# Kernel tuning notes

Measured on AMD Instinct MI355X. Metric: run time of the kernel, lower is better.

Reference implementation:

```python
import jax, jax.numpy as jnp
import numpy as np

TOP_K = 2
POOL = 4  # EfficientSpatialRouter.pool_scale


def silu(v):
    return v * jax.nn.sigmoid(v)


def setup_inputs() -> dict:
    key = jax.random.key(0)
    ks = jax.random.split(key, 6)
    B, C, H, W = 16, 256, 56, 56
    E, O = 4, 256
    hidden = 2 * C            # SimpleExpert expand_ratio=2
    red = max(C // 8, 8)      # router reduced_channels
    x = jax.random.normal(ks[0], (B, C, H, W), jnp.float32)
    router_w1 = jax.random.normal(ks[1], (red, C, 3, 3), jnp.float32) * 0.02
    router_w2 = jax.random.normal(ks[2], (E, red), jnp.float32) * 0.01
    expert_w1 = jax.random.normal(ks[3], (E, hidden, C), jnp.float32) * 0.05
    expert_w2 = jax.random.normal(ks[4], (E, O, hidden), jnp.float32) * 0.03
    shared_w = jax.random.normal(ks[5], (O, C), jnp.float32) * 0.05
    return {"x": x, "router_w1": router_w1, "router_w2": router_w2,
            "expert_w1": expert_w1, "expert_w2": expert_w2, "shared_w": shared_w}


def reference(x, router_w1, router_w2, expert_w1, expert_w2, shared_w):
    # Eval mode: no router noise; BatchNorm with default running stats
    # (mean=0, var=1, gamma=1, beta=0) is the identity, so BNs are omitted.
    B, C, H, W = x.shape
    E = router_w2.shape[0]

    # --- EfficientSpatialRouter ---
    xp = x.reshape(B, C, H // POOL, POOL, W // POOL, POOL).mean(axis=(3, 5))
    h = jax.lax.conv_general_dilated(
        xp, router_w1, window_strides=(1, 1), padding=((1, 1), (1, 1)),
        dimension_numbers=("NCHW", "OIHW", "NCHW"))
    h = silu(h)  # [B, red, H/4, W/4]
    # 1x1 conv to E channels then spatial mean == mean of per-pixel logits
    logits = jnp.einsum("er,brij->be", router_w2, h) / (h.shape[2] * h.shape[3])
    probs = jax.nn.softmax(logits, axis=1)
    topv, topi = jax.lax.top_k(probs, TOP_K)          # [B,k]
    topv = topv / (topv.sum(axis=1, keepdims=True) + 1e-6)

    # --- shared expert (1x1 conv + BN(id) + SiLU) ---
    shared = silu(jnp.einsum("oc,bcij->boij", shared_w, x))

    # --- all SimpleExperts densely (1x1 conv -> SiLU -> 1x1 conv) ---
    hid = silu(jnp.einsum("edc,bcij->bedij", expert_w1, x))   # [B,E,hid,H,W]
    eo = jnp.einsum("eod,bedij->beoij", expert_w2, hid)       # [B,E,O,H,W]

    # --- weighted combine of top-k experts ---
    wdense = jnp.zeros((B, E), x.dtype).at[jnp.arange(B)[:, None], topi].add(topv)
    expert_out = jnp.einsum("be,beoij->boij", wdense, eo)
    return shared + expert_out
```

## Files before the change

### kernel.cpp

```cpp
#include <hip/hip_runtime.h>
#include <hip/hip_bf16.h>

typedef __attribute__((ext_vector_type(8))) short bf16x8;
typedef __attribute__((ext_vector_type(16))) float f32x16;
typedef __attribute__((ext_vector_type(4))) unsigned short ushort4v;

static __device__ __forceinline__ unsigned short f2bf(float f) {
  unsigned u = __float_as_uint(f);
  return (unsigned short)((u + 0x7FFFu + ((u >> 16) & 1u)) >> 16);
}
static __device__ __forceinline__ float silu_f(float v) { return v / (1.f + __expf(-v)); }

__global__ void prep_k(const float* __restrict__ shw, const float* __restrict__ ew1,
                       const float* __restrict__ ew2, const float* __restrict__ x,
                       unsigned short* __restrict__ wshp, unsigned short* __restrict__ w1p,
                       unsigned short* __restrict__ w2p, float* __restrict__ xp) {
  const int bid = blockIdx.x;
  if (bid < 4352) {
    int idx = bid * 256 + threadIdx.x;
    if (idx < 65536) {
      int j = idx;
      int i = j & 7, l = (j >> 3) & 63, ks = (j >> 9) & 15, rb = j >> 13;
      int row = rb * 32 + (l & 31), k = ks * 16 + (l >> 5) * 8 + i;
      wshp[j] = f2bf(shw[row * 256 + k]);
    } else if (idx < 589824) {
      int j = idx - 65536;
      int i = j & 7, l = (j >> 3) & 63, ks = (j >> 9) & 15, rb = (j >> 13) & 15, e = j >> 17;
      int row = rb * 32 + (l & 31), k = ks * 16 + (l >> 5) * 8 + i;
      w1p[j] = f2bf(ew1[((size_t)e * 512 + row) * 256 + k]);
    } else if (idx < 1114112) {
      int j = idx - 589824;
      int i = j & 7, l = (j >> 3) & 63, ks = (j >> 9) & 31, rb = (j >> 14) & 7, e = j >> 17;
      int row = rb * 32 + (l & 31), k = ks * 16 + (l >> 5) * 8 + i;
      w2p[j] = f2bf(ew2[((size_t)e * 256 + row) * 512 + k]);
    }
  } else {
    int idx = (bid - 4352) * 256 + threadIdx.x;
    if (idx >= 16 * 256 * 196) return;
    int pj = idx % 14, tmp = idx / 14, pi = tmp % 14, bc = tmp / 14;
    const float* src = x + (size_t)bc * 3136 + pi * 4 * 56 + pj * 4;
    float s = 0.f;
#pragma unroll
    for (int u = 0; u < 4; ++u) {
      float4 v = *reinterpret_cast<const float4*>(src + u * 56);
      s += v.x + v.y + v.z + v.w;
    }
    xp[idx] = s * 0.0625f;
  }
}

__global__ __launch_bounds__(256) void router_conv_k(const float* __restrict__ xp,
                                                     const float* __restrict__ rw1,
                                                     float* __restrict__ hsum) {
  const int b = blockIdx.x >> 5, r = blockIdx.x & 31;
  __shared__ float wl[2304];
  __shared__ float xl[32][256];
  __shared__ float red[4];
  const int t = threadIdx.x;
  for (int i = t; i < 2304; i += 256) wl[i] = rw1[r * 2304 + i];
  for (int i = t; i < 32 * 256; i += 256) (&xl[0][0])[i] = 0.f;
  const int pi = t / 14, pj = t % 14;
  float acc = 0.f;
  for (int cc = 0; cc < 8; ++cc) {
    __syncthreads();
    for (int i = t; i < 32 * 196; i += 256) {
      int c = i / 196, px = i % 196;
      xl[c][(px / 14 + 1) * 16 + (px % 14 + 1)] =
          xp[((size_t)b * 256 + cc * 32 + c) * 196 + px];
    }
    __syncthreads();
    if (t < 196) {
      for (int c = 0; c < 32; ++c) {
        const float* wp = &wl[(cc * 32 + c) * 9];
        const float* xc = &xl[c][pi * 16 + pj];
#pragma unroll
        for (int u = 0; u < 3; ++u)
#pragma unroll
          for (int v = 0; v < 3; ++v) acc += xc[u * 16 + v] * wp[u * 3 + v];
      }
    }
  }
  float s = (t < 196) ? silu_f(acc) : 0.f;
#pragma unroll
  for (int off = 32; off > 0; off >>= 1) s += __shfl_down(s, off);
  if ((t & 63) == 0) red[t >> 6] = s;
  __syncthreads();
  if (t == 0) hsum[b * 32 + r] = red[0] + red[1] + red[2] + red[3];
}

__global__ void topk_k(const float* __restrict__ hsum, const float* __restrict__ rw2,
                       float* __restrict__ selv, int* __restrict__ sele) {
  const int t = threadIdx.x;
  const int b = t >> 2, e = t & 3;
  float l = 0.f;
#pragma unroll
  for (int r = 0; r < 32; ++r) l += rw2[e * 32 + r] * hsum[b * 32 + r];
  l *= (1.f / 196.f);
  float m = fmaxf(l, __shfl_xor(l, 1));
  m = fmaxf(m, __shfl_xor(m, 2));
  float p = __expf(l - m);
  float sm = p + __shfl_xor(p, 1);
  sm += __shfl_xor(sm, 2);
  float prob = p / sm;
  float p0 = __shfl(prob, (b << 2) | 0);
  float p1 = __shfl(prob, (b << 2) | 1);
  float p2 = __shfl(prob, (b << 2) | 2);
  float p3 = __shfl(prob, (b << 2) | 3);
  if (e == 0) {
    float pr[4] = {p0, p1, p2, p3};
    int i1 = 0;
    for (int i = 1; i < 4; ++i)
      if (pr[i] > pr[i1]) i1 = i;
    int i2 = (i1 == 0) ? 1 : 0;
    for (int i = 0; i < 4; ++i) {
      if (i == i1 || i == i2) continue;
      if (pr[i] > pr[i2]) i2 = i;
    }
    float denom = pr[i1] + pr[i2] + 1e-6f;
    selv[b * 2 + 0] = pr[i1] / denom;
    selv[b * 2 + 1] = pr[i2] / denom;
    sele[b * 2 + 0] = i1;
    sele[b * 2 + 1] = i2;
  }
}

static __device__ __forceinline__ void gemm_k256_p4(
    const unsigned short* __restrict__ A0, const unsigned short* __restrict__ A1,
    const unsigned short* B0, const unsigned short* B1, f32x16 acc[2][2]) {
  bf16x8 a0[4], a1[4], b0[4], b1[4];
#pragma unroll
  for (int s = 0; s < 3; ++s) {
    a0[s] = *reinterpret_cast<const bf16x8*>(A0 + s * 512);
    a1[s] = *reinterpret_cast<const bf16x8*>(A1 + s * 512);
    b0[s] = *reinterpret_cast<const bf16x8*>(B0 + s * 1024);
    b1[s] = *reinterpret_cast<const bf16x8*>(B1 + s * 1024);
  }
#pragma unroll
  for (int ks = 0; ks < 16; ++ks) {
    const int s = ks & 3;
    const int n = (ks + 3) & 3;
    if (ks < 13) {
      a0[n] = *reinterpret_cast<const bf16x8*>(A0 + (ks + 3) * 512);
      a1[n] = *reinterpret_cast<const bf16x8*>(A1 + (ks + 3) * 512);
      b0[n] = *reinterpret_cast<const bf16x8*>(B0 + (ks + 3) * 1024);
      b1[n] = *reinterpret_cast<const bf16x8*>(B1 + (ks + 3) * 1024);
    }
    __builtin_amdgcn_s_setprio(1);
    acc[0][0] = __builtin_amdgcn_mfma_f32_32x32x16_bf16(a0[s], b0[s], acc[0][0], 0, 0, 0);
    acc[0][1] = __builtin_amdgcn_mfma_f32_32x32x16_bf16(a0[s], b1[s], acc[0][1], 0, 0, 0);
    acc[1][0] = __builtin_amdgcn_mfma_f32_32x32x16_bf16(a1[s], b0[s], acc[1][0], 0, 0, 0);
    acc[1][1] = __builtin_amdgcn_mfma_f32_32x32x16_bf16(a1[s], b1[s], acc[1][1], 0, 0, 0);
    __builtin_amdgcn_s_setprio(0);
  }
}

__global__ __launch_bounds__(256, 2) void moe_main_k(
    const float* __restrict__ x, const unsigned short* __restrict__ wshp,
    const unsigned short* __restrict__ w1p, const unsigned short* __restrict__ w2p,
    const float* __restrict__ selv, const int* __restrict__ sele,
    float* __restrict__ out) {
  constexpr int HW = 3136;
  __shared__ __align__(16) unsigned short xs[32 * 64 * 8];
  __shared__ __align__(16) unsigned short hs[32 * 64 * 8];

  const int b = blockIdx.x / 49, tile = blockIdx.x - b * 49;
  const int px0 = tile * 64;
  const int t = threadIdx.x;
  const int w = t >> 6, l = t & 63;
  const int l31 = l & 31, lh = l >> 5;

  {
    const float* xb = x + (size_t)b * 256 * HW + px0 + l;
#pragma unroll
    for (int cg = 0; cg < 8; ++cg) {
      const int c0 = w * 64 + cg * 8;
      alignas(16) unsigned short tmp[8];
#pragma unroll
      for (int i = 0; i < 8; ++i) tmp[i] = f2bf(xb[(size_t)(c0 + i) * HW]);
      *reinterpret_cast<bf16x8*>(&xs[((c0 >> 3) * 64 + l) * 8]) =
          *reinterpret_cast<const bf16x8*>(tmp);
    }
  }

  const unsigned short* xB0 = xs + (lh * 64 + l31) * 8;
  const unsigned short* xB1 = xB0 + 32 * 8;
  const unsigned short* hB0 = hs + (lh * 64 + l31) * 8;
  const unsigned short* hB1 = hB0 + 32 * 8;

  f32x16 oacc[2][2];
#pragma unroll
  for (int i = 0; i < 2; ++i)
#pragma unroll
    for (int j = 0; j < 2; ++j)
#pragma unroll
      for (int r = 0; r < 16; ++r) oacc[i][j][r] = 0.f;

  __syncthreads();

  {
    const unsigned short* A0 = wshp + (size_t)(w * 2) * 16 * 512 + l * 8;
    gemm_k256_p4(A0, A0 + 8192, xB0, xB1, oacc);
  }
#pragma unroll
  for (int i = 0; i < 2; ++i)
#pragma unroll
    for (int j = 0; j < 2; ++j)
#pragma unroll
      for (int r = 0; r < 16; ++r) oacc[i][j][r] = silu_f(oacc[i][j][r]);

#pragma unroll 1
  for (int ei = 0; ei < 2; ++ei) {
    const int e = sele[b * 2 + ei];
    const float v = selv[b * 2 + ei];
#pragma unroll 1
    for (int ph = 0; ph < 2; ++ph) {
      f32x16 hacc[2][2];
#pragma unroll
      for (int i = 0; i < 2; ++i)
#pragma unroll
        for (int j = 0; j < 2; ++j)
#pragma unroll
          for (int r = 0; r < 16; ++r) hacc[i][j][r] = 0.f;
      {
        const unsigned short* A0 =
            w1p + (size_t)(e * 16 + ph * 8 + w * 2) * 16 * 512 + l * 8;
        gemm_k256_p4(A0, A0 + 8192, xB0, xB1, hacc);
      }
      __syncthreads();
#pragma unroll
      for (int rfi = 0; rfi < 2; ++rfi)
#pragma unroll
        for (int cf = 0; cf < 2; ++cf) {
#pragma unroll
          for (int g = 0; g < 4; ++g) {
            alignas(8) unsigned short pk[4];
#pragma unroll
            for (int j = 0; j < 4; ++j)
              pk[j] = f2bf(v * silu_f(hacc[rfi][cf][g * 4 + j]));
            const int kg = w * 8 + rfi * 4 + g;
            const int ui = (kg * 64 + cf * 32 + l31) * 8 + lh * 4;
            *reinterpret_cast<ushort4v*>(&hs[ui]) = *reinterpret_cast<const ushort4v*>(pk);
          }
        }
      __syncthreads();
      {
        const unsigned short* A0 =
            w2p + ((size_t)(e * 8 + w * 2) * 32 + ph * 16) * 512 + l * 8;
        gemm_k256_p4(A0, A0 + 16384, hB0, hB1, oacc);
      }
    }
  }

#pragma unroll
  for (int rfi = 0; rfi < 2; ++rfi)
#pragma unroll
    for (int cf = 0; cf < 2; ++cf)
#pragma unroll
      for (int r = 0; r < 16; ++r) {
        const int o = w * 64 + rfi * 32 + (r & 3) + 8 * (r >> 2) + 4 * lh;
        out[((size_t)b * 256 + o) * HW + px0 + cf * 32 + l31] = oacc[rfi][cf][r];
      }
}

extern "C" void kernel_launch(void* const* d_in, const int* in_sizes, int n_in,
                              void* d_out, int out_size, void* d_ws, size_t ws_size,
                              hipStream_t stream) {
  const float* x = (const float*)d_in[0];
  const float* rw1 = (const float*)d_in[1];
  const float* rw2 = (const float*)d_in[2];
  const float* ew1 = (const float*)d_in[3];
  const float* ew2 = (const float*)d_in[4];
  const float* shw = (const float*)d_in[5];
  float* out = (float*)d_out;
  char* ws = (char*)d_ws;

  float* xp = (float*)(ws);
  float* hsum = (float*)(ws + 3211264);
  float* selv = (float*)(ws + 3213312);
  int* sele = (int*)(ws + 3213440);
  unsigned short* wshp = (unsigned short*)(ws + 3213568);
  unsigned short* w1p = wshp + 65536;
  unsigned short* w2p = w1p + 524288;

  prep_k<<<7488, 256, 0, stream>>>(shw, ew1, ew2, x, wshp, w1p, w2p, xp);
  router_conv_k<<<512, 256, 0, stream>>>(xp, rw1, hsum);
  topk_k<<<1, 64, 0, stream>>>(hsum, rw2, selv, sele);
  moe_main_k<<<784, 256, 0, stream>>>(x, wshp, w1p, w2p, selv, sele, out);
}
```

Measured before the change: 167.6 us.

## Compute four router channels per block and pin MFMA schedule with barriers

The router conv kernel now has each block compute 4 output channels instead of 1. This cuts the grid from 512 to 128 blocks and reuses each staged xp tile and its 9 loaded neighbours across 4 weight sets, with weights read directly from global memory instead of staged in LDS. The main GEMM inner loop also gets sched_barriers around the MFMA group so the compiler keeps the load/MFMA interleaving as written. Fewer router blocks lowers parallelism on a large GPU, and uncached global weight reads may add latency.

```diff
diff --git a/kernel.cpp b/kernel.cpp
--- a/kernel.cpp
+++ b/kernel.cpp
@@ -52,15 +52,13 @@
 __global__ __launch_bounds__(256) void router_conv_k(const float* __restrict__ xp,
                                                      const float* __restrict__ rw1,
                                                      float* __restrict__ hsum) {
-  const int b = blockIdx.x >> 5, r = blockIdx.x & 31;
-  __shared__ float wl[2304];
+  const int b = blockIdx.x >> 3, rg = blockIdx.x & 7;
   __shared__ float xl[32][256];
-  __shared__ float red[4];
+  __shared__ float red[4][4];
   const int t = threadIdx.x;
-  for (int i = t; i < 2304; i += 256) wl[i] = rw1[r * 2304 + i];
+  const int pi = t / 14, pj = t % 14;
+  float acc[4] = {0.f, 0.f, 0.f, 0.f};
   for (int i = t; i < 32 * 256; i += 256) (&xl[0][0])[i] = 0.f;
-  const int pi = t / 14, pj = t % 14;
-  float acc = 0.f;
   for (int cc = 0; cc < 8; ++cc) {
     __syncthreads();
     for (int i = t; i < 32 * 196; i += 256) {
@@ -70,22 +68,31 @@
     }
     __syncthreads();
     if (t < 196) {
+#pragma unroll 4
       for (int c = 0; c < 32; ++c) {
-        const float* wp = &wl[(cc * 32 + c) * 9];
-        const float* xc = &xl[c][pi * 16 + pj];
-#pragma unroll
-        for (int u = 0; u < 3; ++u)
-#pragma unroll
-          for (int v = 0; v < 3; ++v) acc += xc[u * 16 + v] * wp[u * 3 + v];
-      }
-    }
-  }
-  float s = (t < 196) ? silu_f(acc) : 0.f;
-#pragma unroll
-  for (int off = 32; off > 0; off >>= 1) s += __shfl_down(s, off);
-  if ((t & 63) == 0) red[t >> 6] = s;
+        const float* xc = &xl[cc * 32 + c - cc * 32][pi * 16 + pj];
+        const float x0 = xc[0], x1 = xc[1], x2 = xc[2];
+        const float x3 = xc[16], x4 = xc[17], x5 = xc[18];
+        const float x6 = xc[32], x7 = xc[33], x8 = xc[34];
+        const float* wg = rw1 + ((size_t)(rg * 4) * 256 + (cc * 32 + c)) * 9;
+#pragma unroll
+        for (int ri = 0; ri < 4; ++ri) {
+          const float* wp = wg + (size_t)ri * 2304;
+          acc[ri] += x0 * wp[0] + x1 * wp[1] + x2 * wp[2] + x3 * wp[3] + x4 * wp[4] +
+                     x5 * wp[5] + x6 * wp[6] + x7 * wp[7] + x8 * wp[8];
+        }
+      }
+    }
+  }
+#pragma unroll
+  for (int ri = 0; ri < 4; ++ri) {
+    float s = (t < 196) ? silu_f(acc[ri]) : 0.f;
+#pragma unroll
+    for (int off = 32; off > 0; off >>= 1) s += __shfl_down(s, off);
+    if ((t & 63) == 0) red[t >> 6][ri] = s;
+  }
   __syncthreads();
-  if (t == 0) hsum[b * 32 + r] = red[0] + red[1] + red[2] + red[3];
+  if (t < 4) hsum[b * 32 + rg * 4 + t] = red[0][t] + red[1][t] + red[2][t] + red[3][t];
 }
 
 __global__ void topk_k(const float* __restrict__ hsum, const float* __restrict__ rw2,
@@ -135,6 +142,7 @@
     b0[s] = *reinterpret_cast<const bf16x8*>(B0 + s * 1024);
     b1[s] = *reinterpret_cast<const bf16x8*>(B1 + s * 1024);
   }
+  __builtin_amdgcn_sched_barrier(0);
 #pragma unroll
   for (int ks = 0; ks < 16; ++ks) {
     const int s = ks & 3;
@@ -145,12 +153,14 @@
       b0[n] = *reinterpret_cast<const bf16x8*>(B0 + (ks + 3) * 1024);
       b1[n] = *reinterpret_cast<const bf16x8*>(B1 + (ks + 3) * 1024);
     }
+    __builtin_amdgcn_sched_barrier(0);
     __builtin_amdgcn_s_setprio(1);
     acc[0][0] = __builtin_amdgcn_mfma_f32_32x32x16_bf16(a0[s], b0[s], acc[0][0], 0, 0, 0);
     acc[0][1] = __builtin_amdgcn_mfma_f32_32x32x16_bf16(a0[s], b1[s], acc[0][1], 0, 0, 0);
     acc[1][0] = __builtin_amdgcn_mfma_f32_32x32x16_bf16(a1[s], b0[s], acc[1][0], 0, 0, 0);
     acc[1][1] = __builtin_amdgcn_mfma_f32_32x32x16_bf16(a1[s], b1[s], acc[1][1], 0, 0, 0);
     __builtin_amdgcn_s_setprio(0);
+    __builtin_amdgcn_sched_barrier(0);
   }
 }
 
@@ -283,7 +293,7 @@
   unsigned short* w2p = w1p + 524288;
 
   prep_k<<<7488, 256, 0, stream>>>(shw, ew1, ew2, x, wshp, w1p, w2p, xp);
-  router_conv_k<<<512, 256, 0, stream>>>(xp, rw1, hsum);
+  router_conv_k<<<128, 256, 0, stream>>>(xp, rw1, hsum);
   topk_k<<<1, 64, 0, stream>>>(hsum, rw2, selv, sele);
   moe_main_k<<<784, 256, 0, stream>>>(x, wshp, w1p, w2p, selv, sele, out);
 }
```

Result: slower. 223.5 us (+33.4%).

## Software-pipeline expert GEMMs in 128-row chunks with double-buffered hidden LDS

Applied to the files above, without the earlier changes.

The main MoE kernel now works through the hidden dimension in eight 128-row chunks. Each chunk's first-layer GEMM is interleaved with the previous chunk's second-layer GEMM, and the hidden activations go into two alternating LDS buffers. This removes one barrier per phase and lets the two MFMA streams overlap. The first expert chunk is also fused into the shared-expert GEMM pass. Separately, the router conv now gives each thread a 2x2 output block and splits channels across warps, reusing loaded inputs and weights. The explicit register prefetch pipeline and s_setprio hints were dropped, so load latency is left to the compiler and the concurrent streams.

```diff
diff --git a/kernel.cpp b/kernel.cpp
--- a/kernel.cpp
+++ b/kernel.cpp
@@ -10,6 +10,8 @@
   return (unsigned short)((u + 0x7FFFu + ((u >> 16) & 1u)) >> 16);
 }
 static __device__ __forceinline__ float silu_f(float v) { return v / (1.f + __expf(-v)); }
+
+#define MFMA32(a, b, c) __builtin_amdgcn_mfma_f32_32x32x16_bf16((a), (b), (c), 0, 0, 0)
 
 __global__ void prep_k(const float* __restrict__ shw, const float* __restrict__ ew1,
                        const float* __restrict__ ew2, const float* __restrict__ x,
@@ -55,12 +57,14 @@
   const int b = blockIdx.x >> 5, r = blockIdx.x & 31;
   __shared__ float wl[2304];
   __shared__ float xl[32][256];
-  __shared__ float red[4];
+  __shared__ float red[4][196];
+  __shared__ float red2[4];
   const int t = threadIdx.x;
+  const int w = t >> 6, l = t & 63;
   for (int i = t; i < 2304; i += 256) wl[i] = rw1[r * 2304 + i];
   for (int i = t; i < 32 * 256; i += 256) (&xl[0][0])[i] = 0.f;
-  const int pi = t / 14, pj = t % 14;
-  float acc = 0.f;
+  const int ui = (l < 49) ? (l / 7) : 0, uj = (l < 49) ? (l % 7) : 0;
+  float acc[4] = {0.f, 0.f, 0.f, 0.f};
   for (int cc = 0; cc < 8; ++cc) {
     __syncthreads();
     for (int i = t; i < 32 * 196; i += 256) {
@@ -69,23 +73,50 @@
           xp[((size_t)b * 256 + cc * 32 + c) * 196 + px];
     }
     __syncthreads();
-    if (t < 196) {
-      for (int c = 0; c < 32; ++c) {
+    if (l < 49) {
+#pragma unroll 2
+      for (int ci = 0; ci < 8; ++ci) {
+        const int c = w * 8 + ci;
+        float xv[4][4];
+        const float* xb = &xl[c][ui * 32 + uj * 2];
+#pragma unroll
+        for (int dr = 0; dr < 4; ++dr)
+#pragma unroll
+          for (int dc = 0; dc < 4; ++dc) xv[dr][dc] = xb[dr * 16 + dc];
         const float* wp = &wl[(cc * 32 + c) * 9];
-        const float* xc = &xl[c][pi * 16 + pj];
-#pragma unroll
-        for (int u = 0; u < 3; ++u)
-#pragma unroll
-          for (int v = 0; v < 3; ++v) acc += xc[u * 16 + v] * wp[u * 3 + v];
+        float wv[9];
+#pragma unroll
+        for (int j = 0; j < 9; ++j) wv[j] = wp[j];
+#pragma unroll
+        for (int di = 0; di < 2; ++di)
+#pragma unroll
+          for (int dj = 0; dj < 2; ++dj) {
+            float a = acc[di * 2 + dj];
+#pragma unroll
+            for (int du = 0; du < 3; ++du)
+#pragma unroll
+              for (int dv = 0; dv < 3; ++dv)
+                a += xv[di + du][dj + dv] * wv[du * 3 + dv];
+            acc[di * 2 + dj] = a;
+          }
       }
     }
   }
-  float s = (t < 196) ? silu_f(acc) : 0.f;
+  if (l < 49) {
+#pragma unroll
+    for (int k = 0; k < 4; ++k) red[w][(ui * 7 + uj) * 4 + k] = acc[k];
+  }
+  __syncthreads();
+  float s = 0.f;
+  if (t < 196) {
+    float tot = red[0][t] + red[1][t] + red[2][t] + red[3][t];
+    s = silu_f(tot);
+  }
 #pragma unroll
   for (int off = 32; off > 0; off >>= 1) s += __shfl_down(s, off);
-  if ((t & 63) == 0) red[t >> 6] = s;
+  if ((t & 63) == 0) red2[t >> 6] = s;
   __syncthreads();
-  if (t == 0) hsum[b * 32 + r] = red[0] + red[1] + red[2] + red[3];
+  if (t == 0) hsum[b * 32 + r] = red2[0] + red2[1] + red2[2] + red2[3];
 }
 
 __global__ void topk_k(const float* __restrict__ hsum, const float* __restrict__ rw2,
@@ -124,33 +155,20 @@
   }
 }
 
-static __device__ __forceinline__ void gemm_k256_p4(
+template <int NKS>
+static __device__ __forceinline__ void gemm_rf2(
     const unsigned short* __restrict__ A0, const unsigned short* __restrict__ A1,
     const unsigned short* B0, const unsigned short* B1, f32x16 acc[2][2]) {
-  bf16x8 a0[4], a1[4], b0[4], b1[4];
-#pragma unroll
-  for (int s = 0; s < 3; ++s) {
-    a0[s] = *reinterpret_cast<const bf16x8*>(A0 + s * 512);
-    a1[s] = *reinterpret_cast<const bf16x8*>(A1 + s * 512);
-    b0[s] = *reinterpret_cast<const bf16x8*>(B0 + s * 1024);
-    b1[s] = *reinterpret_cast<const bf16x8*>(B1 + s * 1024);
-  }
-#pragma unroll
-  for (int ks = 0; ks < 16; ++ks) {
-    const int s = ks & 3;
-    const int n = (ks + 3) & 3;
-    if (ks < 13) {
-      a0[n] = *reinterpret_cast<const bf16x8*>(A0 + (ks + 3) * 512);
-      a1[n] = *reinterpret_cast<const bf16x8*>(A1 + (ks + 3) * 512);
-      b0[n] = *reinterpret_cast<const bf16x8*>(B0 + (ks + 3) * 1024);
-      b1[n] = *reinterpret_cast<const bf16x8*>(B1 + (ks + 3) * 1024);
-    }
-    __builtin_amdgcn_s_setprio(1);
-    acc[0][0] = __builtin_amdgcn_mfma_f32_32x32x16_bf16(a0[s], b0[s], acc[0][0], 0, 0, 0);
-    acc[0][1] = __builtin_amdgcn_mfma_f32_32x32x16_bf16(a0[s], b1[s], acc[0][1], 0, 0, 0);
-    acc[1][0] = __builtin_amdgcn_mfma_f32_32x32x16_bf16(a1[s], b0[s], acc[1][0], 0, 0, 0);
-    acc[1][1] = __builtin_amdgcn_mfma_f32_32x32x16_bf16(a1[s], b1[s], acc[1][1], 0, 0, 0);
-    __builtin_amdgcn_s_setprio(0);
+#pragma unroll
+  for (int kk = 0; kk < NKS; ++kk) {
+    const bf16x8 a0 = *reinterpret_cast<const bf16x8*>(A0 + kk * 512);
+    const bf16x8 a1 = *reinterpret_cast<const bf16x8*>(A1 + kk * 512);
+    const bf16x8 b0 = *reinterpret_cast<const bf16x8*>(B0 + kk * 1024);
+    const bf16x8 b1 = *reinterpret_cast<const bf16x8*>(B1 + kk * 1024);
+    acc[0][0] = MFMA32(a0, b0, acc[0][0]);
+    acc[0][1] = MFMA32(a0, b1, acc[0][1]);
+    acc[1][0] = MFMA32(a1, b0, acc[1][0]);
+    acc[1][1] = MFMA32(a1, b1, acc[1][1]);
   }
 }
 
@@ -161,7 +179,7 @@
     float* __restrict__ out) {
   constexpr int HW = 3136;
   __shared__ __align__(16) unsigned short xs[32 * 64 * 8];
-  __shared__ __align__(16) unsigned short hs[32 * 64 * 8];
+  __shared__ __align__(16) unsigned short hs[2][16 * 64 * 8];
 
   const int b = blockIdx.x / 49, tile = blockIdx.x - b * 49;
   const int px0 = tile * 64;
@@ -183,23 +201,43 @@
   }
 
   const unsigned short* xB0 = xs + (lh * 64 + l31) * 8;
-  const unsigned short* xB1 = xB0 + 32 * 8;
-  const unsigned short* hB0 = hs + (lh * 64 + l31) * 8;
-  const unsigned short* hB1 = hB0 + 32 * 8;
+  const unsigned short* xB1 = xB0 + 256;
+
+  const int e0 = sele[b * 2 + 0], e1 = sele[b * 2 + 1];
+  const float v0 = selv[b * 2 + 0], v1 = selv[b * 2 + 1];
 
   f32x16 oacc[2][2];
+  f32x16 hacc[2];
 #pragma unroll
   for (int i = 0; i < 2; ++i)
 #pragma unroll
     for (int j = 0; j < 2; ++j)
 #pragma unroll
       for (int r = 0; r < 16; ++r) oacc[i][j][r] = 0.f;
+#pragma unroll
+  for (int j = 0; j < 2; ++j)
+#pragma unroll
+    for (int r = 0; r < 16; ++r) hacc[j][r] = 0.f;
 
   __syncthreads();
 
   {
-    const unsigned short* A0 = wshp + (size_t)(w * 2) * 16 * 512 + l * 8;
-    gemm_k256_p4(A0, A0 + 8192, xB0, xB1, oacc);
+    const unsigned short* A1 = w1p + (size_t)((e0 * 16 + w) * 16) * 512 + l * 8;
+    const unsigned short* As = wshp + (size_t)(w * 2) * 16 * 512 + l * 8;
+#pragma unroll
+    for (int kk = 0; kk < 16; ++kk) {
+      const bf16x8 a1 = *reinterpret_cast<const bf16x8*>(A1 + kk * 512);
+      const bf16x8 s0 = *reinterpret_cast<const bf16x8*>(As + kk * 512);
+      const bf16x8 s1 = *reinterpret_cast<const bf16x8*>(As + 8192 + kk * 512);
+      const bf16x8 b0 = *reinterpret_cast<const bf16x8*>(xB0 + kk * 1024);
+      const bf16x8 b1 = *reinterpret_cast<const bf16x8*>(xB1 + kk * 1024);
+      hacc[0] = MFMA32(a1, b0, hacc[0]);
+      hacc[1] = MFMA32(a1, b1, hacc[1]);
+      oacc[0][0] = MFMA32(s0, b0, oacc[0][0]);
+      oacc[0][1] = MFMA32(s0, b1, oacc[0][1]);
+      oacc[1][0] = MFMA32(s1, b0, oacc[1][0]);
+      oacc[1][1] = MFMA32(s1, b1, oacc[1][1]);
+    }
   }
 #pragma unroll
   for (int i = 0; i < 2; ++i)
@@ -208,47 +246,67 @@
 #pragma unroll
       for (int r = 0; r < 16; ++r) oacc[i][j][r] = silu_f(oacc[i][j][r]);
 
+#pragma unroll
+  for (int cf = 0; cf < 2; ++cf)
+#pragma unroll
+    for (int g = 0; g < 4; ++g) {
+      alignas(8) unsigned short pk[4];
+#pragma unroll
+      for (int j = 0; j < 4; ++j) pk[j] = f2bf(v0 * silu_f(hacc[cf][g * 4 + j]));
+      const int ui2 = ((w * 4 + g) * 64 + cf * 32 + l31) * 8 + lh * 4;
+      *reinterpret_cast<ushort4v*>(&hs[0][ui2]) = *reinterpret_cast<const ushort4v*>(pk);
+    }
+  __syncthreads();
+
 #pragma unroll 1
-  for (int ei = 0; ei < 2; ++ei) {
-    const int e = sele[b * 2 + ei];
-    const float v = selv[b * 2 + ei];
-#pragma unroll 1
-    for (int ph = 0; ph < 2; ++ph) {
-      f32x16 hacc[2][2];
-#pragma unroll
-      for (int i = 0; i < 2; ++i)
-#pragma unroll
-        for (int j = 0; j < 2; ++j)
-#pragma unroll
-          for (int r = 0; r < 16; ++r) hacc[i][j][r] = 0.f;
-      {
-        const unsigned short* A0 =
-            w1p + (size_t)(e * 16 + ph * 8 + w * 2) * 16 * 512 + l * 8;
-        gemm_k256_p4(A0, A0 + 8192, xB0, xB1, hacc);
+  for (int p = 1; p < 8; ++p) {
+    const int e = (p >> 2) ? e1 : e0, ch = p & 3;
+    const int ep = ((p - 1) >> 2) ? e1 : e0, chp = (p - 1) & 3;
+    const float v = (p >> 2) ? v1 : v0;
+    const unsigned short* A1 = w1p + (size_t)((e * 16 + ch * 4 + w) * 16) * 512 + l * 8;
+    const unsigned short* A2 = w2p + ((size_t)(ep * 8 + w * 2) * 32 + chp * 8) * 512 + l * 8;
+    const unsigned short* B2 = hs[(p - 1) & 1] + (lh * 64 + l31) * 8;
+#pragma unroll
+    for (int j = 0; j < 2; ++j)
+#pragma unroll
+      for (int r = 0; r < 16; ++r) hacc[j][r] = 0.f;
+#pragma unroll
+    for (int kk = 0; kk < 16; ++kk) {
+      const bf16x8 a1 = *reinterpret_cast<const bf16x8*>(A1 + kk * 512);
+      const bf16x8 b0 = *reinterpret_cast<const bf16x8*>(xB0 + kk * 1024);
+      const bf16x8 b1 = *reinterpret_cast<const bf16x8*>(xB1 + kk * 1024);
+      hacc[0] = MFMA32(a1, b0, hacc[0]);
+      hacc[1] = MFMA32(a1, b1, hacc[1]);
+      if ((kk & 1) == 0) {
+        const int ks2 = kk >> 1;
+        const bf16x8 a20 = *reinterpret_cast<const bf16x8*>(A2 + ks2 * 512);
+        const bf16x8 a21 = *reinterpret_cast<const bf16x8*>(A2 + 16384 + ks2 * 512);
+        const bf16x8 h0 = *reinterpret_cast<const bf16x8*>(B2 + ks2 * 1024);
+        const bf16x8 h1 = *reinterpret_cast<const bf16x8*>(B2 + 256 + ks2 * 1024);
+        oacc[0][0] = MFMA32(a20, h0, oacc[0][0]);
+        oacc[0][1] = MFMA32(a20, h1, oacc[0][1]);
+        oacc[1][0] = MFMA32(a21, h0, oacc[1][0]);
+        oacc[1][1] = MFMA32(a21, h1, oacc[1][1]);
       }
-      __syncthreads();
-#pragma unroll
-      for (int rfi = 0; rfi < 2; ++rfi)
-#pragma unroll
-        for (int cf = 0; cf < 2; ++cf) {
-#pragma unroll
-          for (int g = 0; g < 4; ++g) {
-            alignas(8) unsigned short pk[4];
-#pragma unroll
-            for (int j = 0; j < 4; ++j)
-              pk[j] = f2bf(v * silu_f(hacc[rfi][cf][g * 4 + j]));
-            const int kg = w * 8 + rfi * 4 + g;
-            const int ui = (kg * 64 + cf * 32 + l31) * 8 + lh * 4;
-            *reinterpret_cast<ushort4v*>(&hs[ui]) = *reinterpret_cast<const ushort4v*>(pk);
-          }
-        }
-      __syncthreads();
-      {
-        const unsigned short* A0 =
-            w2p + ((size_t)(e * 8 + w * 2) * 32 + ph * 16) * 512 + l * 8;
-        gemm_k256_p4(A0, A0 + 16384, hB0, hB1, oacc);
+    }
+#pragma unroll
+    for (int cf = 0; cf < 2; ++cf)
+#pragma unroll
+      for (int g = 0; g < 4; ++g) {
+        alignas(8) unsigned short pk[4];
+#pragma unroll
+        for (int j = 0; j < 4; ++j) pk[j] = f2bf(v * silu_f(hacc[cf][g * 4 + j]));
+        const int ui2 = ((w * 4 + g) * 64 + cf * 32 + l31) * 8 + lh * 4;
+        *reinterpret_cast<ushort4v*>(&hs[p & 1][ui2]) =
+            *reinterpret_cast<const ushort4v*>(pk);
       }
-    }
+    __syncthreads();
+  }
+
+  {
+    const unsigned short* A2 = w2p + ((size_t)(e1 * 8 + w * 2) * 32 + 3 * 8) * 512 + l * 8;
+    const unsigned short* B2 = hs[1] + (lh * 64 + l31) * 8;
+    gemm_rf2<8>(A2, A2 + 16384, B2, B2 + 256, oacc);
   }
 
 #pragma unroll
```

Result: slower. 188.7 us (+12.6%).

## Warp-specialize MoE kernel into hidden-producer and output-consumer waves with double-buffered LDS

Applied to the files above, without the earlier changes.

Doubles the block to 512 threads and splits the waves by role. Four waves compute the first expert GEMM plus SiLU into a double-buffered LDS hidden tile, in chunks covering both selected experts. The other four waves compute the shared expert, then consume each hidden chunk in the second GEMM, so the two expert GEMMs overlap through a barrier handshake. A-fragment loads are batched ahead of MFMA bursts with sched barriers. The launch bound of 4 blocks per CU tightly caps registers, and the 16-fragment batch in the producer waves risks spills.

```diff
diff --git a/kernel.cpp b/kernel.cpp
--- a/kernel.cpp
+++ b/kernel.cpp
@@ -10,6 +10,9 @@
   return (unsigned short)((u + 0x7FFFu + ((u >> 16) & 1u)) >> 16);
 }
 static __device__ __forceinline__ float silu_f(float v) { return v / (1.f + __expf(-v)); }
+
+#define MFMA32(a, b, c) __builtin_amdgcn_mfma_f32_32x32x16_bf16((a), (b), (c), 0, 0, 0)
+#define SBAR() __builtin_amdgcn_sched_barrier(0x102)
 
 __global__ void prep_k(const float* __restrict__ shw, const float* __restrict__ ew1,
                        const float* __restrict__ ew2, const float* __restrict__ x,
@@ -124,44 +127,14 @@
   }
 }
 
-static __device__ __forceinline__ void gemm_k256_p4(
-    const unsigned short* __restrict__ A0, const unsigned short* __restrict__ A1,
-    const unsigned short* B0, const unsigned short* B1, f32x16 acc[2][2]) {
-  bf16x8 a0[4], a1[4], b0[4], b1[4];
-#pragma unroll
-  for (int s = 0; s < 3; ++s) {
-    a0[s] = *reinterpret_cast<const bf16x8*>(A0 + s * 512);
-    a1[s] = *reinterpret_cast<const bf16x8*>(A1 + s * 512);
-    b0[s] = *reinterpret_cast<const bf16x8*>(B0 + s * 1024);
-    b1[s] = *reinterpret_cast<const bf16x8*>(B1 + s * 1024);
-  }
-#pragma unroll
-  for (int ks = 0; ks < 16; ++ks) {
-    const int s = ks & 3;
-    const int n = (ks + 3) & 3;
-    if (ks < 13) {
-      a0[n] = *reinterpret_cast<const bf16x8*>(A0 + (ks + 3) * 512);
-      a1[n] = *reinterpret_cast<const bf16x8*>(A1 + (ks + 3) * 512);
-      b0[n] = *reinterpret_cast<const bf16x8*>(B0 + (ks + 3) * 1024);
-      b1[n] = *reinterpret_cast<const bf16x8*>(B1 + (ks + 3) * 1024);
-    }
-    __builtin_amdgcn_s_setprio(1);
-    acc[0][0] = __builtin_amdgcn_mfma_f32_32x32x16_bf16(a0[s], b0[s], acc[0][0], 0, 0, 0);
-    acc[0][1] = __builtin_amdgcn_mfma_f32_32x32x16_bf16(a0[s], b1[s], acc[0][1], 0, 0, 0);
-    acc[1][0] = __builtin_amdgcn_mfma_f32_32x32x16_bf16(a1[s], b0[s], acc[1][0], 0, 0, 0);
-    acc[1][1] = __builtin_amdgcn_mfma_f32_32x32x16_bf16(a1[s], b1[s], acc[1][1], 0, 0, 0);
-    __builtin_amdgcn_s_setprio(0);
-  }
-}
-
-__global__ __launch_bounds__(256, 2) void moe_main_k(
+__global__ __launch_bounds__(512, 4) void moe_main_k(
     const float* __restrict__ x, const unsigned short* __restrict__ wshp,
     const unsigned short* __restrict__ w1p, const unsigned short* __restrict__ w2p,
     const float* __restrict__ selv, const int* __restrict__ sele,
     float* __restrict__ out) {
   constexpr int HW = 3136;
   __shared__ __align__(16) unsigned short xs[32 * 64 * 8];
-  __shared__ __align__(16) unsigned short hs[32 * 64 * 8];
+  __shared__ __align__(16) unsigned short hs[2][16 * 64 * 8];
 
   const int b = blockIdx.x / 49, tile = blockIdx.x - b * 49;
   const int px0 = tile * 64;
@@ -172,8 +145,8 @@
   {
     const float* xb = x + (size_t)b * 256 * HW + px0 + l;
 #pragma unroll
-    for (int cg = 0; cg < 8; ++cg) {
-      const int c0 = w * 64 + cg * 8;
+    for (int cg = 0; cg < 4; ++cg) {
+      const int c0 = w * 32 + cg * 8;
       alignas(16) unsigned short tmp[8];
 #pragma unroll
       for (int i = 0; i < 8; ++i) tmp[i] = f2bf(xb[(size_t)(c0 + i) * HW]);
@@ -182,84 +155,144 @@
     }
   }
 
+  const int e0 = sele[b * 2 + 0], e1 = sele[b * 2 + 1];
+  const float v0 = selv[b * 2 + 0], v1 = selv[b * 2 + 1];
+
   const unsigned short* xB0 = xs + (lh * 64 + l31) * 8;
-  const unsigned short* xB1 = xB0 + 32 * 8;
-  const unsigned short* hB0 = hs + (lh * 64 + l31) * 8;
-  const unsigned short* hB1 = hB0 + 32 * 8;
-
-  f32x16 oacc[2][2];
-#pragma unroll
-  for (int i = 0; i < 2; ++i)
-#pragma unroll
-    for (int j = 0; j < 2; ++j)
-#pragma unroll
-      for (int r = 0; r < 16; ++r) oacc[i][j][r] = 0.f;
+  const unsigned short* xB1 = xB0 + 256;
 
   __syncthreads();
 
-  {
-    const unsigned short* A0 = wshp + (size_t)(w * 2) * 16 * 512 + l * 8;
-    gemm_k256_p4(A0, A0 + 8192, xB0, xB1, oacc);
-  }
-#pragma unroll
-  for (int i = 0; i < 2; ++i)
-#pragma unroll
-    for (int j = 0; j < 2; ++j)
-#pragma unroll
-      for (int r = 0; r < 16; ++r) oacc[i][j][r] = silu_f(oacc[i][j][r]);
-
+  if (w < 4) {
+    f32x16 hacc[2];
 #pragma unroll 1
-  for (int ei = 0; ei < 2; ++ei) {
-    const int e = sele[b * 2 + ei];
-    const float v = selv[b * 2 + ei];
+    for (int q = 0; q < 8; ++q) {
+      const int p = q;
+      const int e = (p >> 2) ? e1 : e0, ch = p & 3;
+      const float v = (p >> 2) ? v1 : v0;
+      const unsigned short* A1 =
+          w1p + (size_t)((e * 16 + ch * 4 + w) * 16) * 512 + l * 8;
+#pragma unroll
+      for (int j = 0; j < 2; ++j)
+#pragma unroll
+        for (int r = 0; r < 16; ++r) hacc[j][r] = 0.f;
+      bf16x8 af[16];
+#pragma unroll
+      for (int j = 0; j < 16; ++j)
+        af[j] = *reinterpret_cast<const bf16x8*>(A1 + j * 512);
+      SBAR();
+      __builtin_amdgcn_s_setprio(1);
+#pragma unroll
+      for (int j = 0; j < 16; ++j) {
+        const bf16x8 b0 = *reinterpret_cast<const bf16x8*>(xB0 + j * 1024);
+        const bf16x8 b1 = *reinterpret_cast<const bf16x8*>(xB1 + j * 1024);
+        hacc[0] = MFMA32(af[j], b0, hacc[0]);
+        hacc[1] = MFMA32(af[j], b1, hacc[1]);
+      }
+      __builtin_amdgcn_s_setprio(0);
+      ushort4v pk[2][4];
+#pragma unroll
+      for (int cf = 0; cf < 2; ++cf)
+#pragma unroll
+        for (int g = 0; g < 4; ++g) {
+          alignas(8) unsigned short tmp[4];
+#pragma unroll
+          for (int j = 0; j < 4; ++j) tmp[j] = f2bf(v * silu_f(hacc[cf][g * 4 + j]));
+          pk[cf][g] = *reinterpret_cast<const ushort4v*>(tmp);
+        }
+#pragma unroll
+      for (int cf = 0; cf < 2; ++cf)
+#pragma unroll
+        for (int g = 0; g < 4; ++g) {
+          const int ui2 = ((w * 4 + g) * 64 + cf * 32 + l31) * 8 + lh * 4;
+          *reinterpret_cast<ushort4v*>(&hs[p & 1][ui2]) = pk[cf][g];
+        }
+      __syncthreads();
+    }
+    __syncthreads();
+  } else {
+    const int wc = w - 4;
+    f32x16 oacc[2][2];
+#pragma unroll
+    for (int i = 0; i < 2; ++i)
+#pragma unroll
+      for (int j = 0; j < 2; ++j)
+#pragma unroll
+        for (int r = 0; r < 16; ++r) oacc[i][j][r] = 0.f;
+
+    {
+      const unsigned short* As = wshp + (size_t)(wc * 2) * 16 * 512 + l * 8;
+#pragma unroll
+      for (int g = 0; g < 4; ++g) {
+        bf16x8 a0f[4], a1f[4];
+#pragma unroll
+        for (int j = 0; j < 4; ++j) {
+          a0f[j] = *reinterpret_cast<const bf16x8*>(As + (g * 4 + j) * 512);
+          a1f[j] = *reinterpret_cast<const bf16x8*>(As + 8192 + (g * 4 + j) * 512);
+        }
+        SBAR();
+        __builtin_amdgcn_s_setprio(1);
+#pragma unroll
+        for (int j = 0; j < 4; ++j) {
+          const bf16x8 b0 = *reinterpret_cast<const bf16x8*>(xB0 + (g * 4 + j) * 1024);
+          const bf16x8 b1 = *reinterpret_cast<const bf16x8*>(xB1 + (g * 4 + j) * 1024);
+          oacc[0][0] = MFMA32(a0f[j], b0, oacc[0][0]);
+          oacc[0][1] = MFMA32(a0f[j], b1, oacc[0][1]);
+          oacc[1][0] = MFMA32(a1f[j], b0, oacc[1][0]);
+          oacc[1][1] = MFMA32(a1f[j], b1, oacc[1][1]);
+        }
+        __builtin_amdgcn_s_setprio(0);
+      }
+    }
+#pragma unroll
+    for (int i = 0; i < 2; ++i)
+#pragma unroll
+      for (int j = 0; j < 2; ++j)
+#pragma unroll
+        for (int r = 0; r < 16; ++r) oacc[i][j][r] = silu_f(oacc[i][j][r]);
+
+    __syncthreads();
 #pragma unroll 1
-    for (int ph = 0; ph < 2; ++ph) {
-      f32x16 hacc[2][2];
-#pragma unroll
-      for (int i = 0; i < 2; ++i)
-#pragma unroll
-        for (int j = 0; j < 2; ++j)
-#pragma unroll
-          for (int r = 0; r < 16; ++r) hacc[i][j][r] = 0.f;
-      {
-        const unsigned short* A0 =
-            w1p + (size_t)(e * 16 + ph * 8 + w * 2) * 16 * 512 + l * 8;
-        gemm_k256_p4(A0, A0 + 8192, xB0, xB1, hacc);
+    for (int q = 0; q < 8; ++q) {
+      const int e = (q >> 2) ? e1 : e0, ch = q & 3;
+      const unsigned short* A2 =
+          w2p + ((size_t)(e * 8 + wc * 2) * 32 + ch * 8) * 512 + l * 8;
+      const unsigned short* hB0 = hs[q & 1] + (lh * 64 + l31) * 8;
+      const unsigned short* hB1 = hB0 + 256;
+#pragma unroll
+      for (int g = 0; g < 2; ++g) {
+        bf16x8 a0f[4], a1f[4];
+#pragma unroll
+        for (int j = 0; j < 4; ++j) {
+          a0f[j] = *reinterpret_cast<const bf16x8*>(A2 + (g * 4 + j) * 512);
+          a1f[j] = *reinterpret_cast<const bf16x8*>(A2 + 16384 + (g * 4 + j) * 512);
+        }
+        SBAR();
+        __builtin_amdgcn_s_setprio(1);
+#pragma unroll
+        for (int j = 0; j < 4; ++j) {
+          const bf16x8 h0 = *reinterpret_cast<const bf16x8*>(hB0 + (g * 4 + j) * 1024);
+          const bf16x8 h1 = *reinterpret_cast<const bf16x8*>(hB1 + (g * 4 + j) * 1024);
+          oacc[0][0] = MFMA32(a0f[j], h0, oacc[0][0]);
+          oacc[0][1] = MFMA32(a0f[j], h1, oacc[0][1]);
+          oacc[1][0] = MFMA32(a1f[j], h0, oacc[1][0]);
+          oacc[1][1] = MFMA32(a1f[j], h1, oacc[1][1]);
+        }
+        __builtin_amdgcn_s_setprio(0);
       }
       __syncthreads();
-#pragma unroll
-      for (int rfi = 0; rfi < 2; ++rfi)
-#pragma unroll
-        for (int cf = 0; cf < 2; ++cf) {
-#pragma unroll
-          for (int g = 0; g < 4; ++g) {
-            alignas(8) unsigned short pk[4];
-#pragma unroll
-            for (int j = 0; j < 4; ++j)
-              pk[j] = f2bf(v * silu_f(hacc[rfi][cf][g * 4 + j]));
-            const int kg = w * 8 + rfi * 4 + g;
-            const int ui = (kg * 64 + cf * 32 + l31) * 8 + lh * 4;
-            *reinterpret_cast<ushort4v*>(&hs[ui]) = *reinterpret_cast<const ushort4v*>(pk);
-          }
-        }
-      __syncthreads();
-      {
-        const unsigned short* A0 =
-            w2p + ((size_t)(e * 8 + w * 2) * 32 + ph * 16) * 512 + l * 8;
-        gemm_k256_p4(A0, A0 + 16384, hB0, hB1, oacc);
-      }
-    }
-  }
-
-#pragma unroll
-  for (int rfi = 0; rfi < 2; ++rfi)
-#pragma unroll
-    for (int cf = 0; cf < 2; ++cf)
-#pragma unroll
-      for (int r = 0; r < 16; ++r) {
-        const int o = w * 64 + rfi * 32 + (r & 3) + 8 * (r >> 2) + 4 * lh;
-        out[((size_t)b * 256 + o) * HW + px0 + cf * 32 + l31] = oacc[rfi][cf][r];
-      }
+    }
+
+#pragma unroll
+    for (int rfi = 0; rfi < 2; ++rfi)
+#pragma unroll
+      for (int cf = 0; cf < 2; ++cf)
+#pragma unroll
+        for (int r = 0; r < 16; ++r) {
+          const int o = wc * 64 + rfi * 32 + (r & 3) + 8 * (r >> 2) + 4 * lh;
+          out[((size_t)b * 256 + o) * HW + px0 + cf * 32 + l31] = oacc[rfi][cf][r];
+        }
+  }
 }
 
 extern "C" void kernel_launch(void* const* d_in, const int* in_sizes, int n_in,
@@ -285,5 +318,5 @@
   prep_k<<<7488, 256, 0, stream>>>(shw, ew1, ew2, x, wshp, w1p, w2p, xp);
   router_conv_k<<<512, 256, 0, stream>>>(xp, rw1, hsum);
   topk_k<<<1, 64, 0, stream>>>(hsum, rw2, selv, sele);
-  moe_main_k<<<784, 256, 0, stream>>>(x, wshp, w1p, w2p, selv, sele, out);
-}
+  moe_main_k<<<784, 512, 0, stream>>>(x, wshp, w1p, w2p, selv, sele, out);
+}
```

Measured after the change: 169.4 us. About the same (+1.1%).
